# Kernel optimization log

Measured on AMD Instinct MI355X. Metric: run time of the kernel, lower is better.

Reference implementation:

```python
import jax, jax.numpy as jnp
import numpy as np

# dims
N = 10000      # nodes
E = 320000     # edges (avg degree 32)
NS = 64        # hidden 0e scalar channels
NV = 64        # hidden 1o vector channels
EMB = 32       # node-attr embedding dim
NTYPES = 20    # max_atom_types
NB = 8         # number_of_basis (bessel)
RH = 16        # radial_neurons
L = 2          # layers
CUT = 3.5      # max_radius
NNEIGH = 32.0  # num_neighbors normalization
H = 0.1        # residual step size


def smooth_cutoff(u):
    # e3nn example smooth_cutoff applied to x/max_radius
    v = 2.0 * (u - 1.0)
    y = 0.5 * (1.0 - jnp.cos(jnp.pi * v))
    y = jnp.where(v > 0.0, 0.0, y)
    y = jnp.where(v < -1.0, 1.0, y)
    return y


def setup_inputs() -> dict:
    key = jax.random.key(0)
    ks = jax.random.split(key, 10)
    x = jax.random.normal(ks[0], (N, 6), jnp.float32)
    batch = jnp.zeros((N,), jnp.int32)
    node_attr = jax.random.randint(ks[1], (N,), 0, NTYPES)
    edge_src = jax.random.randint(ks[2], (E,), 0, N)
    # avoid self-loops (zero edge length -> NaN in sh / bessel)
    off = jax.random.randint(ks[3], (E,), 1, N)
    edge_dst = (edge_src + off) % N
    embed_table = 0.1 * jax.random.normal(ks[4], (NTYPES, EMB), jnp.float32)
    Ku = jax.random.normal(ks[5], (2, NV), jnp.float32)          # uplift (made semi-unitary via QR)
    W_sc_s = 0.05 * jax.random.normal(ks[6], (L, NS, EMB, NS + NV), jnp.float32)  # self-connection TP: scalars
    W_sc_v = 0.05 * jax.random.normal(ks[7], (L, NV, EMB, NV), jnp.float32)       # self-connection TP: vectors
    Wr1 = 0.3 * jax.random.normal(ks[8], (L, NB, RH), jnp.float32)
    br1 = jnp.zeros((L, RH), jnp.float32)
    Wr2 = 0.3 * jax.random.normal(ks[9], (L, RH, 4 * NV), jnp.float32)
    br2 = jnp.zeros((L, 4 * NV), jnp.float32)
    return {"x": x, "batch": batch, "node_attr": node_attr, "edge_src": edge_src,
            "edge_dst": edge_dst, "embed_table": embed_table, "Ku": Ku,
            "W_sc_s": W_sc_s, "W_sc_v": W_sc_v, "Wr1": Wr1, "br1": br1,
            "Wr2": Wr2, "br2": br2}


def reference(x, batch, node_attr, edge_src, edge_dst, embed_table, Ku,
              W_sc_s, W_sc_v, Wr1, br1, Wr2, br2):
    n = x.shape[0]
    a = embed_table[node_attr]                     # [n, EMB] node-attr embedding (0e scalars)
    # make uplift semi-unitary: Q^T Q = I_2
    Q, _ = jnp.linalg.qr(Ku.T)                     # [NV, 2]
    U = Q.T                                        # uplift [2, NV]
    x_v = x.reshape(n, 2, 3)                       # 2x1o: position, velocity
    y_s = jnp.zeros((n, NS), x.dtype)              # uplift has no 1o->0e path
    y_v = jnp.einsum('ncd,ch->nhd', x_v, U)        # [n, NV, 3]
    nfreq = jnp.arange(1, NB + 1, dtype=x.dtype)
    inv_deg = 1.0 / np.sqrt(NNEIGH)
    for l in range(L):
        pos = x_v[:, 0, :]
        ev = pos[edge_src] - pos[edge_dst]                          # [E, 3]
        elen = jnp.linalg.norm(ev, axis=1)                          # [E]
        sh = jnp.sqrt(3.0) * ev / elen[:, None]                     # 1x1o SH, component norm
        # bessel radial basis, scaled by sqrt(NB)
        bess = (jnp.sqrt(2.0 / CUT) * jnp.sin(jnp.pi * nfreq * elen[:, None] / CUT)
                / elen[:, None]) * np.sqrt(NB)                      # [E, NB]
        ea = smooth_cutoff(elen / CUT)[:, None] * sh                # edge_attr [E, 3]
        # radial MLP -> per-edge tensor-product weights (4 paths x NV channels)
        w = jax.nn.silu(bess @ Wr1[l] + br1[l]) @ Wr2[l] + br2[l]   # [E, 4*NV]
        wA, wB, wC, wD = jnp.split(w, 4, axis=1)
        s_src = y_s[edge_src]                                       # [E, NS]
        v_src = y_v[edge_src]                                       # [E, NV, 3]
        # TP paths: 0e x 1o -> 1o ; 1o x 1o -> 1o (cross) ; 1o x 1o -> 0e (dot, feats + gates)
        msg_v = (wA[:, :, None] * s_src[:, :, None] * ea[:, None, :]
                 + wC[:, :, None] * jnp.cross(v_src, ea[:, None, :]))  # [E, NV, 3]
        dots = jnp.einsum('evd,ed->ev', v_src, ea)                  # [E, NV]
        msg_s = jnp.concatenate([wB * dots, wD * dots], axis=1)     # [E, NS+NV]
        agg_s = jax.ops.segment_sum(msg_s, edge_dst, num_segments=n) * inv_deg
        agg_v = (jax.ops.segment_sum(msg_v.reshape(msg_v.shape[0], -1), edge_dst,
                                     num_segments=n).reshape(n, NV, 3) * inv_deg)
        # self-connection: fully-connected TP with node-attr scalars
        sc_s = jnp.einsum('ns,ne,seo->no', y_s, a, W_sc_s[l])       # [n, NS+NV]
        sc_v = jnp.einsum('nvd,ne,veu->nud', y_v, a, W_sc_v[l])     # [n, NV, 3]
        out_s = sc_s + agg_s
        out_v = sc_v + agg_v
        # gate: silu on scalar feats, sigmoid gates scale the vectors
        y_s = y_s + H * jax.nn.silu(out_s[:, :NS])
        y_v = y_v + H * jax.nn.sigmoid(out_s[:, NS:])[:, :, None] * out_v
        # project back to 2x1o
        x_v = jnp.einsum('nhd,hc->ncd', y_v, Q)
    return x_v.reshape(n, 6)
```

## Files before the change

kernel.cpp:

```cpp
#include <hip/hip_runtime.h>
#include <math.h>

#define NSC 64
#define NVC 64
#define EMB 32
#define NTYPES 20
#define NB 8
#define RH 16
#define LAYERS 2
#define CUTV 3.5f
#define HSTEP 0.1f

__device__ __forceinline__ unsigned short f2bf(float f)
{
  unsigned u = __float_as_uint(f);
  unsigned r = (u + 0x7FFFu + ((u >> 16) & 1u)) >> 16;
  return (unsigned short)r;
}
__device__ __forceinline__ float bf2f(unsigned short u)
{
  return __uint_as_float(((unsigned)u) << 16);
}

__device__ __forceinline__ float wave_sum(float t)
{
  #pragma unroll
  for (int mm = 1; mm < 64; mm <<= 1) t += __shfl_xor(t, mm, 64);
  return t;
}

__global__ void qr_kernel(const float* __restrict__ Ku, float* __restrict__ Q)
{
  const int i = threadIdx.x;
  float a0 = Ku[i], a1 = Ku[64 + i];
  const float xn2 = wave_sum((i >= 1) ? a0 * a0 : 0.f);
  const float alpha = __shfl(a0, 0, 64);
  const float beta0 = -copysignf(sqrtf(alpha * alpha + xn2), alpha);
  const float tau0 = (beta0 - alpha) / beta0;
  const float inv0 = 1.f / (alpha - beta0);
  const float v0 = (i == 0) ? 1.f : a0 * inv0;
  const float w = wave_sum(v0 * a1);
  a1 -= tau0 * w * v0;
  const float alpha1 = __shfl(a1, 1, 64);
  const float xn2b = wave_sum((i >= 2) ? a1 * a1 : 0.f);
  const float beta1 = -copysignf(sqrtf(alpha1 * alpha1 + xn2b), alpha1);
  const float tau1 = (beta1 - alpha1) / beta1;
  const float inv1 = 1.f / (alpha1 - beta1);
  const float v1 = (i == 0) ? 0.f : ((i == 1) ? 1.f : a1 * inv1);
  const float t1v = ((i == 1) ? 1.f : 0.f) - tau1 * v1;
  const float d = wave_sum(v0 * t1v);
  Q[i * 2 + 0] = ((i == 0) ? 1.f : 0.f) - tau0 * v0;
  Q[i * 2 + 1] = t1v - tau0 * d * v0;
}

__global__ void init_state(const float* __restrict__ x, const float* __restrict__ Qm,
                           ushort4* __restrict__ st0, int* __restrict__ cnt, int n)
{
  const int i = blockIdx.x * 256 + threadIdx.x;
  const int node = i >> 6, lane = i & 63;
  if (node < n) {
    const float q0 = Qm[lane * 2 + 0], q1 = Qm[lane * 2 + 1];
    const float* xp = x + (size_t)node * 6;
    st0[i] = make_ushort4(0,
                          f2bf(xp[0] * q0 + xp[3] * q1),
                          f2bf(xp[1] * q0 + xp[4] * q1),
                          f2bf(xp[2] * q0 + xp[5] * q1));
  }
  if (i < n) cnt[i] = 0;
}

__global__ void hist_kernel(const int* __restrict__ edst, int* __restrict__ cnt, int m)
{
  const int e = blockIdx.x * 256 + threadIdx.x;
  if (e < m) atomicAdd(&cnt[edst[e]], 1);
}

__global__ void scan_kernel(int* cnt, int* off, int n)
{
  __shared__ int lds[1024];
  const int t = threadIdx.x;
  const int CH = (n + 1023) >> 10;
  const int base = t * CH;
  int local[16];
  int run = 0;
  for (int j = 0; j < CH; ++j) {
    int v = (base + j < n) ? cnt[base + j] : 0;
    local[j] = run;
    run += v;
  }
  lds[t] = run;
  __syncthreads();
  for (int s = 1; s < 1024; s <<= 1) {
    int v = (t >= s) ? lds[t - s] : 0;
    __syncthreads();
    lds[t] += v;
    __syncthreads();
  }
  const int excl = lds[t] - run;
  for (int j = 0; j < CH; ++j) {
    if (base + j < n) {
      int o = excl + local[j];
      off[base + j] = o;
      cnt[base + j] = o;
    }
  }
  if (t == 1023) off[n] = lds[1023];
}

__global__ void scatter_kernel(const int* __restrict__ esrc, const int* __restrict__ edst,
                               int* __restrict__ cursor,
                               int* __restrict__ esrc_s, int* __restrict__ edst_s, int m)
{
  const int e = blockIdx.x * 256 + threadIdx.x;
  if (e < m) {
    const int d = edst[e];
    int p = atomicAdd(&cursor[d], 1);
    esrc_s[p] = esrc[e];
    edst_s[p] = d;
  }
}

__global__ void type_weights(const float* __restrict__ embed,
                             const float* __restrict__ Wss,
                             const float* __restrict__ Wsv,
                             float* __restrict__ Ws, float* __restrict__ Wv,
                             int total_s, int total_v)
{
  const int i = blockIdx.x * 256 + threadIdx.x;
  if (i < total_s) {
    const int bid = i >> 13;
    const int p = i & 8191;
    const int l = bid / NTYPES, t = bid % NTYPES;
    const int s = p >> 7, o = p & 127;
    const float* ar = embed + t * EMB;
    const float* wp = Wss + ((size_t)(l * 64 + s) * EMB) * 128 + o;
    float acc = 0.f;
    #pragma unroll
    for (int e = 0; e < EMB; ++e) acc = fmaf(ar[e], wp[e * 128], acc);
    Ws[i] = acc;
  } else {
    const int j = i - total_s;
    if (j < total_v) {
      const int bid = j >> 12;
      const int p = j & 4095;
      const int l = bid / NTYPES, t = bid % NTYPES;
      const int v = p >> 6, u = p & 63;
      const float* ar = embed + t * EMB;
      const float* wp = Wsv + ((size_t)(l * 64 + v) * EMB) * 64 + u;
      float acc = 0.f;
      #pragma unroll
      for (int e = 0; e < EMB; ++e) acc = fmaf(ar[e], wp[e * 64], acc);
      Wv[j] = acc;
    }
  }
}

__global__ void transpose_wr2(const float* __restrict__ Wr2, float* __restrict__ Wt)
{
  const int t = blockIdx.x * 256 + threadIdx.x;
  if (t >= LAYERS * 256) return;
  const int l = t >> 8, ch = t & 255;
  #pragma unroll
  for (int j = 0; j < RH; ++j)
    Wt[(size_t)l * 4096 + ch * RH + j] = Wr2[(size_t)l * 4096 + j * 256 + ch];
}

__global__ void edge_geom(const float* __restrict__ xv,
                          const int* __restrict__ esrc_s, const int* __restrict__ edst_s,
                          const float* __restrict__ Wr1l, const float* __restrict__ br1l,
                          float4* __restrict__ ea4, float* __restrict__ hidb, int m)
{
  const int k = blockIdx.x * 256 + threadIdx.x;
  if (k >= m) return;
  const int s = esrc_s[k], d = edst_s[k];
  const float ex = xv[(size_t)s * 6 + 0] - xv[(size_t)d * 6 + 0];
  const float ey = xv[(size_t)s * 6 + 1] - xv[(size_t)d * 6 + 1];
  const float ez = xv[(size_t)s * 6 + 2] - xv[(size_t)d * 6 + 2];
  const float len = sqrtf(ex * ex + ey * ey + ez * ez);
  const float invl = 1.f / len;
  const float u = len * (1.f / CUTV);
  const float arg = (float)M_PI * u;
  float sa, ca;
  __sincosf(arg, &sa, &ca);
  const float vv = 2.f * (u - 1.f);
  float cut = 0.5f * (1.f - (2.f * ca * ca - 1.f));
  cut = (vv > 0.f) ? 0.f : cut;
  cut = (vv < -1.f) ? 1.f : cut;
  const float cc = cut * 1.7320508075688772f * invl;
  ea4[k] = make_float4(cc * ex, cc * ey, cc * ez, 0.f);
  float bess[NB];
  const float amp = 2.1380899352993948f * invl;
  const float twoc = 2.f * ca;
  float sm1 = 0.f, scur = sa;
  #pragma unroll
  for (int kk = 0; kk < NB; ++kk) {
    bess[kk] = amp * scur;
    const float snext = twoc * scur - sm1;
    sm1 = scur; scur = snext;
  }
  float hid[RH];
  #pragma unroll
  for (int j = 0; j < RH; ++j) {
    float h = br1l[j];
    #pragma unroll
    for (int kk = 0; kk < NB; ++kk) h = fmaf(bess[kk], Wr1l[kk * RH + j], h);
    hid[j] = h / (1.f + expf(-h));
  }
  float4* hp = (float4*)(hidb + (size_t)k * 16);
  hp[0] = make_float4(hid[0],  hid[1],  hid[2],  hid[3]);
  hp[1] = make_float4(hid[4],  hid[5],  hid[6],  hid[7]);
  hp[2] = make_float4(hid[8],  hid[9],  hid[10], hid[11]);
  hp[3] = make_float4(hid[12], hid[13], hid[14], hid[15]);
}

#define MLPW                                                                  \
  float w = bias;                                                             \
  w = fmaf(g1.x, W0.x, w); w = fmaf(g1.y, W0.y, w);                           \
  w = fmaf(g1.z, W0.z, w); w = fmaf(g1.w, W0.w, w);                           \
  w = fmaf(g2.x, W1.x, w); w = fmaf(g2.y, W1.y, w);                           \
  w = fmaf(g2.z, W1.z, w); w = fmaf(g2.w, W1.w, w);                           \
  w = fmaf(g3.x, W2.x, w); w = fmaf(g3.y, W2.y, w);                           \
  w = fmaf(g3.z, W2.z, w); w = fmaf(g3.w, W2.w, w);                           \
  w = fmaf(g4.x, W3.x, w); w = fmaf(g4.y, W3.y, w);                           \
  w = fmaf(g4.z, W3.z, w); w = fmaf(g4.w, W3.w, w);

#define EDGE_PIPELINE(QSTMT)                                                  \
  for (int k = k0; k < k1; k += 8) {                                          \
    int idx[8];                                                               \
    float msk[8];                                                             \
    _Pragma("unroll")                                                         \
    for (int j = 0; j < 8; ++j) {                                             \
      idx[j] = (k + j < k1) ? (k + j) : (k1 - 1);                             \
      msk[j] = (k + j < k1) ? 1.f : 0.f;                                      \
    }                                                                         \
    ushort4 stP[8];                                                           \
    _Pragma("unroll")                                                         \
    for (int j = 0; j < 8; ++j)                                               \
      stP[j] = st_in[(size_t)esrc_s[idx[j]] * 64 + lane];                     \
    float4 eaP[8];                                                            \
    _Pragma("unroll")                                                         \
    for (int j = 0; j < 8; ++j) eaP[j] = ea4[idx[j]];                         \
    _Pragma("unroll")                                                         \
    for (int j = 0; j < 8; ++j) {                                             \
      const float4* hb = (const float4*)(hidb + (size_t)idx[j] * 16);         \
      const float4 g1 = hb[0], g2 = hb[1], g3 = hb[2], g4 = hb[3];            \
      const float4 stc = make_float4(bf2f(stP[j].x), bf2f(stP[j].y),          \
                                     bf2f(stP[j].z), bf2f(stP[j].w));         \
      const float4 ea = eaP[j];                                               \
      MLPW;                                                                   \
      w *= msk[j];                                                            \
      QSTMT                                                                   \
    }                                                                         \
  }

__global__ __launch_bounds__(256, 3) void gather_update(
    const int* __restrict__ off, const int* __restrict__ esrc_s,
    const float4* __restrict__ ea4, const float* __restrict__ hidb,
    const ushort4* __restrict__ st_in, const int* __restrict__ nattr,
    const float* __restrict__ Ws, const float* __restrict__ Wv,
    const float* __restrict__ Wtl, const float* __restrict__ br2l,
    const float* __restrict__ Qm,
    ushort4* __restrict__ st_out, float* __restrict__ xv_out, int n)
{
  __shared__ float eAx[64], eAy[64], eAz[64], eCx[64], eCy[64], eCz[64];
  __shared__ float eB[64], eD[64];
  __shared__ float oP[4][5][64];
  const int lane = threadIdx.x & 63;
  const int wid = threadIdx.x >> 6;
  const int node = blockIdx.x;

  const int chg = (wid << 6) + lane;
  const float* wp = Wtl + (size_t)chg * RH;
  const float4 W0 = *(const float4*)wp;
  const float4 W1 = *(const float4*)(wp + 4);
  const float4 W2 = *(const float4*)(wp + 8);
  const float4 W3 = *(const float4*)(wp + 12);
  const float bias = br2l[chg];

  float a0 = 0.f, a1 = 0.f, a2 = 0.f;
  const int k0 = off[node], k1 = off[node + 1];
  if (k0 < k1) {
    if (wid == 0) {
      EDGE_PIPELINE({
        const float t = w * stc.x;
        a0 = fmaf(t, ea.x, a0); a1 = fmaf(t, ea.y, a1); a2 = fmaf(t, ea.z, a2);
      })
    } else if (wid == 1) {
      EDGE_PIPELINE({
        const float dt = stc.y * ea.x + stc.z * ea.y + stc.w * ea.z;
        a0 = fmaf(w, dt, a0);
      })
    } else if (wid == 2) {
      EDGE_PIPELINE({
        a0 = fmaf(w, stc.z * ea.z - stc.w * ea.y, a0);
        a1 = fmaf(w, stc.w * ea.x - stc.y * ea.z, a1);
        a2 = fmaf(w, stc.y * ea.y - stc.z * ea.x, a2);
      })
    } else {
      EDGE_PIPELINE({
        const float dt = stc.y * ea.x + stc.z * ea.y + stc.w * ea.z;
        a0 = fmaf(w, dt, a0);
      })
    }
  }
  if (wid == 0)      { eAx[lane] = a0; eAy[lane] = a1; eAz[lane] = a2; }
  else if (wid == 1) { eB[lane] = a0; }
  else if (wid == 2) { eCx[lane] = a0; eCy[lane] = a1; eCz[lane] = a2; }
  else               { eD[lane] = a0; }

  const int ty = nattr[node];
  const float* WsT = Ws + (size_t)ty * 8192;
  const float* WvT = Wv + (size_t)ty * 4096;
  const ushort4 ownb = st_in[(size_t)node * 64 + lane];
  const float own_s = bf2f(ownb.x), own_x = bf2f(ownb.y),
              own_y = bf2f(ownb.z), own_z = bf2f(ownb.w);
  float oS1 = 0.f, oS2 = 0.f, oV0 = 0.f, oV1 = 0.f, oV2 = 0.f;
  const int s20 = wid << 4;
  #pragma unroll 4
  for (int s2 = s20; s2 < s20 + 16; ++s2) {
    const float yss = __shfl(own_s, s2, 64);
    const float b0 = __shfl(own_x, s2, 64);
    const float b1 = __shfl(own_y, s2, 64);
    const float b2 = __shfl(own_z, s2, 64);
    oS1 = fmaf(yss, WsT[s2 * 128 + lane], oS1);
    oS2 = fmaf(yss, WsT[s2 * 128 + 64 + lane], oS2);
    const float wvv = WvT[s2 * 64 + lane];
    oV0 = fmaf(b0, wvv, oV0);
    oV1 = fmaf(b1, wvv, oV1);
    oV2 = fmaf(b2, wvv, oV2);
  }
  oP[wid][0][lane] = oS1; oP[wid][1][lane] = oS2;
  oP[wid][2][lane] = oV0; oP[wid][3][lane] = oV1; oP[wid][4][lane] = oV2;
  __syncthreads();

  if (wid == 0) {
    const float inv_deg = 0.17677669529663687f;
    const float aS1 = eB[lane], aS2 = eD[lane];
    const float aV0 = eAx[lane] + eCx[lane];
    const float aV1 = eAy[lane] + eCy[lane];
    const float aV2 = eAz[lane] + eCz[lane];
    float s1 = 0.f, s2v = 0.f, v0 = 0.f, v1 = 0.f, v2 = 0.f;
    #pragma unroll
    for (int q = 0; q < 4; ++q) {
      s1 += oP[q][0][lane]; s2v += oP[q][1][lane];
      v0 += oP[q][2][lane]; v1 += oP[q][3][lane]; v2 += oP[q][4][lane];
    }
    const float outS1 = s1 + aS1 * inv_deg;
    const float outS2 = s2v + aS2 * inv_deg;
    const float sig1 = 1.f / (1.f + expf(-outS1));
    const float gate = 1.f / (1.f + expf(-outS2));
    const float ysn = own_s + HSTEP * outS1 * sig1;
    const float gf = HSTEP * gate;
    const float yvn0 = own_x + gf * (v0 + aV0 * inv_deg);
    const float yvn1 = own_y + gf * (v1 + aV1 * inv_deg);
    const float yvn2 = own_z + gf * (v2 + aV2 * inv_deg);
    st_out[(size_t)node * 64 + lane] =
        make_ushort4(f2bf(ysn), f2bf(yvn0), f2bf(yvn1), f2bf(yvn2));

    const float q0 = Qm[lane * 2 + 0], q1 = Qm[lane * 2 + 1];
    float pr[6] = { yvn0 * q0, yvn1 * q0, yvn2 * q0,
                    yvn0 * q1, yvn1 * q1, yvn2 * q1 };
    #pragma unroll
    for (int mm = 1; mm < 64; mm <<= 1) {
      #pragma unroll
      for (int i = 0; i < 6; ++i) pr[i] += __shfl_xor(pr[i], mm, 64);
    }
    if (lane == 0) {
      #pragma unroll
      for (int i = 0; i < 6; ++i) xv_out[(size_t)node * 6 + i] = pr[i];
    }
  }
}

extern "C" void kernel_launch(void* const* d_in, const int* in_sizes, int n_in,
                              void* d_out, int out_size, void* d_ws, size_t ws_size,
                              hipStream_t stream)
{
  const float* x     = (const float*)d_in[0];
  const int*   nattr = (const int*)d_in[2];
  const int*   esrc  = (const int*)d_in[3];
  const int*   edst  = (const int*)d_in[4];
  const float* embed = (const float*)d_in[5];
  const float* Ku    = (const float*)d_in[6];
  const float* Wss   = (const float*)d_in[7];
  const float* Wsv   = (const float*)d_in[8];
  const float* Wr1   = (const float*)d_in[9];
  const float* br1   = (const float*)d_in[10];
  const float* Wr2   = (const float*)d_in[11];
  const float* br2   = (const float*)d_in[12];
  const int n = in_sizes[0] / 6;
  const int m = in_sizes[3];

  char* p = (char*)d_ws;
  auto alloc = [&](size_t bytes) -> char* {
    char* r = p;
    p += (bytes + 255) & ~(size_t)255;
    return r;
  };
  int*     off    = (int*)alloc((size_t)(n + 1) * 4);
  int*     cursor = (int*)alloc((size_t)n * 4);
  int*     esrc_s = (int*)alloc((size_t)m * 4);
  int*     edst_s = (int*)alloc((size_t)m * 4);
  float*   Q      = (float*)alloc(128 * 4);
  float*   Ws     = (float*)alloc((size_t)LAYERS * NTYPES * 64 * 128 * 4);
  float*   Wv     = (float*)alloc((size_t)LAYERS * NTYPES * 64 * 64 * 4);
  ushort4* st0    = (ushort4*)alloc((size_t)n * 64 * 8);
  ushort4* st1    = (ushort4*)alloc((size_t)n * 64 * 8);
  float*   xvb    = (float*)alloc((size_t)n * 6 * 4);
  float4*  ea4    = (float4*)alloc((size_t)m * 16);
  float*   hidb   = (float*)alloc((size_t)m * 16 * 4);
  float*   Wt     = (float*)alloc((size_t)LAYERS * 4096 * 4);

  const int total_s = LAYERS * NTYPES * 64 * 128;
  const int total_v = LAYERS * NTYPES * 64 * 64;

  qr_kernel<<<1, 64, 0, stream>>>(Ku, Q);
  init_state<<<(n * 64 + 255) / 256, 256, 0, stream>>>(x, Q, st0, cursor, n);
  hist_kernel<<<(m + 255) / 256, 256, 0, stream>>>(edst, cursor, m);
  scan_kernel<<<1, 1024, 0, stream>>>(cursor, off, n);
  scatter_kernel<<<(m + 255) / 256, 256, 0, stream>>>(esrc, edst, cursor, esrc_s, edst_s, m);
  type_weights<<<(total_s + total_v + 255) / 256, 256, 0, stream>>>(
      embed, Wss, Wsv, Ws, Wv, total_s, total_v);
  transpose_wr2<<<2, 256, 0, stream>>>(Wr2, Wt);

  const float* xv_cur = x;
  const ushort4* st_cur = st0;
  ushort4* st_nxt = st1;
  for (int l = 0; l < LAYERS; ++l) {
    edge_geom<<<(m + 255) / 256, 256, 0, stream>>>(
        xv_cur, esrc_s, edst_s, Wr1 + l * NB * RH, br1 + l * RH, ea4, hidb, m);
    float* xv_out = (l == LAYERS - 1) ? (float*)d_out : xvb;
    gather_update<<<n, 256, 0, stream>>>(
        off, esrc_s, ea4, hidb, st_cur, nattr,
        Ws + (size_t)l * NTYPES * 8192, Wv + (size_t)l * NTYPES * 4096,
        Wt + (size_t)l * 4096, br2 + l * 256, Q,
        st_nxt, xv_out, n);
    xv_cur = xv_out;
    ushort4* ts = (ushort4*)st_cur; st_cur = st_nxt; st_nxt = ts;
  }
}
```

Before: 320.5 us.

## Process two nodes per block with two waves per node sharing edge gathers

The gather/update kernel now handles two nodes per 256-thread block. Each wave computes two radial-MLP output channel groups per edge instead of one, so every gathered neighbour state row and edge attribute is loaded by two waves rather than four. The self-connection loop is split across two waves instead of four, and the final combine sums only two partials. Each wave now holds two weight vectors in registers and the launch bound drops from three to two blocks, which trades occupancy for less redundant gather traffic.

Result: slower. 459.5 us (+43.4%).

```diff
diff --git a/kernel.cpp b/kernel.cpp
--- a/kernel.cpp
+++ b/kernel.cpp
@@ -213,16 +213,26 @@
   hp[3] = make_float4(hid[12], hid[13], hid[14], hid[15]);
 }
 
-#define MLPW                                                                  \
-  float w = bias;                                                             \
-  w = fmaf(g1.x, W0.x, w); w = fmaf(g1.y, W0.y, w);                           \
-  w = fmaf(g1.z, W0.z, w); w = fmaf(g1.w, W0.w, w);                           \
-  w = fmaf(g2.x, W1.x, w); w = fmaf(g2.y, W1.y, w);                           \
-  w = fmaf(g2.z, W1.z, w); w = fmaf(g2.w, W1.w, w);                           \
-  w = fmaf(g3.x, W2.x, w); w = fmaf(g3.y, W2.y, w);                           \
-  w = fmaf(g3.z, W2.z, w); w = fmaf(g3.w, W2.w, w);                           \
-  w = fmaf(g4.x, W3.x, w); w = fmaf(g4.y, W3.y, w);                           \
-  w = fmaf(g4.z, W3.z, w); w = fmaf(g4.w, W3.w, w);
+#define MLP2                                                                  \
+  float wA = biasA, wB = biasB;                                               \
+  wA = fmaf(g1.x, A0.x, wA); wA = fmaf(g1.y, A0.y, wA);                       \
+  wA = fmaf(g1.z, A0.z, wA); wA = fmaf(g1.w, A0.w, wA);                       \
+  wA = fmaf(g2.x, A1.x, wA); wA = fmaf(g2.y, A1.y, wA);                       \
+  wA = fmaf(g2.z, A1.z, wA); wA = fmaf(g2.w, A1.w, wA);                       \
+  wA = fmaf(g3.x, A2.x, wA); wA = fmaf(g3.y, A2.y, wA);                       \
+  wA = fmaf(g3.z, A2.z, wA); wA = fmaf(g3.w, A2.w, wA);                       \
+  wA = fmaf(g4.x, A3.x, wA); wA = fmaf(g4.y, A3.y, wA);                       \
+  wA = fmaf(g4.z, A3.z, wA); wA = fmaf(g4.w, A3.w, wA);                       \
+  float wBv = biasB;                                                          \
+  (void)wB;                                                                   \
+  wBv = fmaf(g1.x, B0.x, wBv); wBv = fmaf(g1.y, B0.y, wBv);                   \
+  wBv = fmaf(g1.z, B0.z, wBv); wBv = fmaf(g1.w, B0.w, wBv);                   \
+  wBv = fmaf(g2.x, B1.x, wBv); wBv = fmaf(g2.y, B1.y, wBv);                   \
+  wBv = fmaf(g2.z, B1.z, wBv); wBv = fmaf(g2.w, B1.w, wBv);                   \
+  wBv = fmaf(g3.x, B2.x, wBv); wBv = fmaf(g3.y, B2.y, wBv);                   \
+  wBv = fmaf(g3.z, B2.z, wBv); wBv = fmaf(g3.w, B2.w, wBv);                   \
+  wBv = fmaf(g4.x, B3.x, wBv); wBv = fmaf(g4.y, B3.y, wBv);                   \
+  wBv = fmaf(g4.z, B3.z, wBv); wBv = fmaf(g4.w, B3.w, wBv);
 
 #define EDGE_PIPELINE(QSTMT)                                                  \
   for (int k = k0; k < k1; k += 8) {                                          \
@@ -237,23 +247,21 @@
     _Pragma("unroll")                                                         \
     for (int j = 0; j < 8; ++j)                                               \
       stP[j] = st_in[(size_t)esrc_s[idx[j]] * 64 + lane];                     \
-    float4 eaP[8];                                                            \
-    _Pragma("unroll")                                                         \
-    for (int j = 0; j < 8; ++j) eaP[j] = ea4[idx[j]];                         \
     _Pragma("unroll")                                                         \
     for (int j = 0; j < 8; ++j) {                                             \
       const float4* hb = (const float4*)(hidb + (size_t)idx[j] * 16);         \
       const float4 g1 = hb[0], g2 = hb[1], g3 = hb[2], g4 = hb[3];            \
+      const float4 ea = ea4[idx[j]];                                          \
       const float4 stc = make_float4(bf2f(stP[j].x), bf2f(stP[j].y),          \
                                      bf2f(stP[j].z), bf2f(stP[j].w));         \
-      const float4 ea = eaP[j];                                               \
-      MLPW;                                                                   \
-      w *= msk[j];                                                            \
+      MLP2;                                                                   \
+      wA *= msk[j];                                                           \
+      wBv *= msk[j];                                                          \
       QSTMT                                                                   \
     }                                                                         \
   }
 
-__global__ __launch_bounds__(256, 3) void gather_update(
+__global__ __launch_bounds__(256, 2) void gather_update(
     const int* __restrict__ off, const int* __restrict__ esrc_s,
     const float4* __restrict__ ea4, const float* __restrict__ hidb,
     const ushort4* __restrict__ st_in, const int* __restrict__ nattr,
@@ -262,89 +270,90 @@
     const float* __restrict__ Qm,
     ushort4* __restrict__ st_out, float* __restrict__ xv_out, int n)
 {
-  __shared__ float eAx[64], eAy[64], eAz[64], eCx[64], eCy[64], eCz[64];
-  __shared__ float eB[64], eD[64];
+  __shared__ float pV0[4][64], pV1[4][64], pV2[4][64], pS[4][64];
   __shared__ float oP[4][5][64];
   const int lane = threadIdx.x & 63;
   const int wid = threadIdx.x >> 6;
-  const int node = blockIdx.x;
-
-  const int chg = (wid << 6) + lane;
-  const float* wp = Wtl + (size_t)chg * RH;
-  const float4 W0 = *(const float4*)wp;
-  const float4 W1 = *(const float4*)(wp + 4);
-  const float4 W2 = *(const float4*)(wp + 8);
-  const float4 W3 = *(const float4*)(wp + 12);
-  const float bias = br2l[chg];
-
-  float a0 = 0.f, a1 = 0.f, a2 = 0.f;
-  const int k0 = off[node], k1 = off[node + 1];
-  if (k0 < k1) {
-    if (wid == 0) {
-      EDGE_PIPELINE({
-        const float t = w * stc.x;
-        a0 = fmaf(t, ea.x, a0); a1 = fmaf(t, ea.y, a1); a2 = fmaf(t, ea.z, a2);
-      })
-    } else if (wid == 1) {
-      EDGE_PIPELINE({
-        const float dt = stc.y * ea.x + stc.z * ea.y + stc.w * ea.z;
-        a0 = fmaf(w, dt, a0);
-      })
-    } else if (wid == 2) {
-      EDGE_PIPELINE({
-        a0 = fmaf(w, stc.z * ea.z - stc.w * ea.y, a0);
-        a1 = fmaf(w, stc.w * ea.x - stc.y * ea.z, a1);
-        a2 = fmaf(w, stc.y * ea.y - stc.z * ea.x, a2);
-      })
-    } else {
-      EDGE_PIPELINE({
-        const float dt = stc.y * ea.x + stc.z * ea.y + stc.w * ea.z;
-        a0 = fmaf(w, dt, a0);
-      })
-    }
-  }
-  if (wid == 0)      { eAx[lane] = a0; eAy[lane] = a1; eAz[lane] = a2; }
-  else if (wid == 1) { eB[lane] = a0; }
-  else if (wid == 2) { eCx[lane] = a0; eCy[lane] = a1; eCz[lane] = a2; }
-  else               { eD[lane] = a0; }
-
-  const int ty = nattr[node];
-  const float* WsT = Ws + (size_t)ty * 8192;
-  const float* WvT = Wv + (size_t)ty * 4096;
-  const ushort4 ownb = st_in[(size_t)node * 64 + lane];
-  const float own_s = bf2f(ownb.x), own_x = bf2f(ownb.y),
-              own_y = bf2f(ownb.z), own_z = bf2f(ownb.w);
-  float oS1 = 0.f, oS2 = 0.f, oV0 = 0.f, oV1 = 0.f, oV2 = 0.f;
-  const int s20 = wid << 4;
-  #pragma unroll 4
-  for (int s2 = s20; s2 < s20 + 16; ++s2) {
-    const float yss = __shfl(own_s, s2, 64);
-    const float b0 = __shfl(own_x, s2, 64);
-    const float b1 = __shfl(own_y, s2, 64);
-    const float b2 = __shfl(own_z, s2, 64);
-    oS1 = fmaf(yss, WsT[s2 * 128 + lane], oS1);
-    oS2 = fmaf(yss, WsT[s2 * 128 + 64 + lane], oS2);
-    const float wvv = WvT[s2 * 64 + lane];
-    oV0 = fmaf(b0, wvv, oV0);
-    oV1 = fmaf(b1, wvv, oV1);
-    oV2 = fmaf(b2, wvv, oV2);
-  }
-  oP[wid][0][lane] = oS1; oP[wid][1][lane] = oS2;
-  oP[wid][2][lane] = oV0; oP[wid][3][lane] = oV1; oP[wid][4][lane] = oV2;
+  const int half = wid & 1;
+  const int node = blockIdx.x * 2 + (wid >> 1);
+  const bool active = node < n;
+
+  const int chA = (half << 7) + lane;
+  const float* wpA = Wtl + (size_t)chA * RH;
+  const float* wpB = Wtl + (size_t)(chA + 64) * RH;
+  const float4 A0 = *(const float4*)wpA;
+  const float4 A1 = *(const float4*)(wpA + 4);
+  const float4 A2 = *(const float4*)(wpA + 8);
+  const float4 A3 = *(const float4*)(wpA + 12);
+  const float4 B0 = *(const float4*)wpB;
+  const float4 B1 = *(const float4*)(wpB + 4);
+  const float4 B2 = *(const float4*)(wpB + 8);
+  const float4 B3 = *(const float4*)(wpB + 12);
+  const float biasA = br2l[chA], biasB = br2l[chA + 64];
+
+  float a0 = 0.f, a1 = 0.f, a2 = 0.f, aS = 0.f;
+  float own_s = 0.f, own_x = 0.f, own_y = 0.f, own_z = 0.f;
+  if (active) {
+    const int k0 = off[node], k1 = off[node + 1];
+    if (k0 < k1) {
+      if (half == 0) {
+        EDGE_PIPELINE({
+          const float t = wA * stc.x;
+          a0 = fmaf(t, ea.x, a0); a1 = fmaf(t, ea.y, a1); a2 = fmaf(t, ea.z, a2);
+          const float dt = stc.y * ea.x + stc.z * ea.y + stc.w * ea.z;
+          aS = fmaf(wBv, dt, aS);
+        })
+      } else {
+        EDGE_PIPELINE({
+          a0 = fmaf(wA, stc.z * ea.z - stc.w * ea.y, a0);
+          a1 = fmaf(wA, stc.w * ea.x - stc.y * ea.z, a1);
+          a2 = fmaf(wA, stc.y * ea.y - stc.z * ea.x, a2);
+          const float dt = stc.y * ea.x + stc.z * ea.y + stc.w * ea.z;
+          aS = fmaf(wBv, dt, aS);
+        })
+      }
+    }
+    pV0[wid][lane] = a0; pV1[wid][lane] = a1; pV2[wid][lane] = a2;
+    pS[wid][lane] = aS;
+
+    const int ty = nattr[node];
+    const float* WsT = Ws + (size_t)ty * 8192;
+    const float* WvT = Wv + (size_t)ty * 4096;
+    const ushort4 ownb = st_in[(size_t)node * 64 + lane];
+    own_s = bf2f(ownb.x); own_x = bf2f(ownb.y);
+    own_y = bf2f(ownb.z); own_z = bf2f(ownb.w);
+    float oS1 = 0.f, oS2 = 0.f, oV0 = 0.f, oV1 = 0.f, oV2 = 0.f;
+    const int s20 = half << 5;
+    #pragma unroll 4
+    for (int s2 = s20; s2 < s20 + 32; ++s2) {
+      const float yss = __shfl(own_s, s2, 64);
+      const float b0 = __shfl(own_x, s2, 64);
+      const float b1 = __shfl(own_y, s2, 64);
+      const float b2 = __shfl(own_z, s2, 64);
+      oS1 = fmaf(yss, WsT[s2 * 128 + lane], oS1);
+      oS2 = fmaf(yss, WsT[s2 * 128 + 64 + lane], oS2);
+      const float wvv = WvT[s2 * 64 + lane];
+      oV0 = fmaf(b0, wvv, oV0);
+      oV1 = fmaf(b1, wvv, oV1);
+      oV2 = fmaf(b2, wvv, oV2);
+    }
+    oP[wid][0][lane] = oS1; oP[wid][1][lane] = oS2;
+    oP[wid][2][lane] = oV0; oP[wid][3][lane] = oV1; oP[wid][4][lane] = oV2;
+  }
   __syncthreads();
 
-  if (wid == 0) {
+  if (active && half == 0) {
     const float inv_deg = 0.17677669529663687f;
-    const float aS1 = eB[lane], aS2 = eD[lane];
-    const float aV0 = eAx[lane] + eCx[lane];
-    const float aV1 = eAy[lane] + eCy[lane];
-    const float aV2 = eAz[lane] + eCz[lane];
-    float s1 = 0.f, s2v = 0.f, v0 = 0.f, v1 = 0.f, v2 = 0.f;
-    #pragma unroll
-    for (int q = 0; q < 4; ++q) {
-      s1 += oP[q][0][lane]; s2v += oP[q][1][lane];
-      v0 += oP[q][2][lane]; v1 += oP[q][3][lane]; v2 += oP[q][4][lane];
-    }
+    const int w2 = wid + 1;
+    const float aS1 = pS[wid][lane], aS2 = pS[w2][lane];
+    const float aV0 = pV0[wid][lane] + pV0[w2][lane];
+    const float aV1 = pV1[wid][lane] + pV1[w2][lane];
+    const float aV2 = pV2[wid][lane] + pV2[w2][lane];
+    const float s1 = oP[wid][0][lane] + oP[w2][0][lane];
+    const float s2v = oP[wid][1][lane] + oP[w2][1][lane];
+    const float v0 = oP[wid][2][lane] + oP[w2][2][lane];
+    const float v1 = oP[wid][3][lane] + oP[w2][3][lane];
+    const float v2 = oP[wid][4][lane] + oP[w2][4][lane];
     const float outS1 = s1 + aS1 * inv_deg;
     const float outS2 = s2v + aS2 * inv_deg;
     const float sig1 = 1.f / (1.f + expf(-outS1));
@@ -430,7 +439,7 @@
     edge_geom<<<(m + 255) / 256, 256, 0, stream>>>(
         xv_cur, esrc_s, edst_s, Wr1 + l * NB * RH, br1 + l * RH, ea4, hidb, m);
     float* xv_out = (l == LAYERS - 1) ? (float*)d_out : xvb;
-    gather_update<<<n, 256, 0, stream>>>(
+    gather_update<<<(n + 1) / 2, 256, 0, stream>>>(
         off, esrc_s, ea4, hidb, st_cur, nattr,
         Ws + (size_t)l * NTYPES * 8192, Wv + (size_t)l * NTYPES * 4096,
         Wt + (size_t)l * 4096, br2 + l * 256, Q,
```
